# Kernel optimization log

Measured on AMD Instinct MI355X. Metric: run time of the kernel, lower is better.

## Reference

```python
import jax, jax.numpy as jnp
import numpy as np

KH = KW = 3
STRIDE = 1
PAD = 1
DIL = 1


def setup_inputs() -> dict:
    key = jax.random.key(0)
    k0, k1, k2, k3 = jax.random.split(key, 4)
    B, C, H, W = 4, 64, 128, 128
    Cout = 64
    K = KH * KW
    x = jax.random.normal(k0, (B, C, H, W), jnp.float32)
    # main deform-conv weight [Cout, C, KH, KW]
    weight = jax.random.normal(k1, (Cout, C, KH, KW), jnp.float32) * (1.0 / np.sqrt(C * K))
    bias = jax.random.normal(k2, (Cout,), jnp.float32) * 0.01
    # offset-generating conv: 2*K output channels (dy,dx per kernel tap), deform_groups=1
    offset_weight = jax.random.normal(k3, (2 * K, C, KH, KW), jnp.float32) * 0.01
    offset_bias = jnp.zeros((2 * K,), jnp.float32)
    return {"x": x, "weight": weight, "bias": bias,
            "offset_weight": offset_weight, "offset_bias": offset_bias}


def _conv(x, w, b):
    out = jax.lax.conv_general_dilated(
        x, w, (STRIDE, STRIDE), [(PAD, PAD), (PAD, PAD)],
        rhs_dilation=(DIL, DIL), dimension_numbers=("NCHW", "OIHW", "NCHW"))
    return out + b[None, :, None, None]


def _deform_conv(x, weight, bias, offset_weight, offset_bias):
    B, C, H, W = x.shape
    K = KH * KW
    # offsets from sibling conv: [B, 2K, Ho, Wo], layout (k, [dy, dx]) interleaved
    offs = _conv(x, offset_weight, offset_bias)
    Ho, Wo = offs.shape[2], offs.shape[3]
    offs = offs.reshape(B, K, 2, Ho, Wo)
    dy, dx = offs[:, :, 0], offs[:, :, 1]          # [B, K, Ho, Wo]

    # base sampling grid: output pixel origin + dilated kernel tap + learned offset
    base_h = (jnp.arange(Ho) * STRIDE - PAD).astype(x.dtype)
    base_w = (jnp.arange(Wo) * STRIDE - PAD).astype(x.dtype)
    ky, kx = jnp.meshgrid(jnp.arange(KH) * DIL, jnp.arange(KW) * DIL, indexing="ij")
    ky = ky.reshape(K).astype(x.dtype)
    kx = kx.reshape(K).astype(x.dtype)
    py = base_h[None, None, :, None] + ky[None, :, None, None] + dy   # [B,K,Ho,Wo]
    px = base_w[None, None, None, :] + kx[None, :, None, None] + dx

    y0 = jnp.floor(py)
    x0 = jnp.floor(px)
    ly = py - y0   # fractional weights
    lx = px - x0
    y0i = y0.astype(jnp.int32)
    x0i = x0.astype(jnp.int32)

    x_flat = x.reshape(B, C, H * W)

    def gather(yi, xi):
        # zero padding outside the image
        valid = (yi >= 0) & (yi < H) & (xi >= 0) & (xi < W)
        yc = jnp.clip(yi, 0, H - 1)
        xc = jnp.clip(xi, 0, W - 1)
        idx = (yc * W + xc).reshape(B, -1)          # [B, K*Ho*Wo]
        g = jax.vmap(lambda f, i: f[:, i])(x_flat, idx)  # [B, C, K*Ho*Wo]
        g = g.reshape(B, C, K, Ho, Wo)
        return g * valid[:, None].astype(x.dtype)

    v00 = gather(y0i,     x0i)
    v01 = gather(y0i,     x0i + 1)
    v10 = gather(y0i + 1, x0i)
    v11 = gather(y0i + 1, x0i + 1)

    wy = ly[:, None]   # [B,1,K,Ho,Wo]
    wx = lx[:, None]
    patches = (v00 * (1 - wy) * (1 - wx) + v01 * (1 - wy) * wx
               + v10 * wy * (1 - wx) + v11 * wy * wx)   # [B,C,K,Ho,Wo]

    Cout = weight.shape[0]
    out = jnp.einsum("bckhw,ock->bohw", patches, weight.reshape(Cout, C, K))
    return out + bias[None, :, None, None]


def reference(x, weight, bias, offset_weight, offset_bias):
    return _deform_conv(x, weight, bias, offset_weight, offset_bias)
```

## Files before the change

### kernel.cpp

```cpp
#include <hip/hip_runtime.h>

#define B_   4
#define C_   64
#define H_   128
#define W_   128
#define OC_  64
#define K_   9
#define OCH_ 18
#define CK_  576

#define S_    104
#define WCOLS 768
#define XSW   72
#define XSH2  5
#define XSC2  (XSH2*XSW)
#define CHF   (8*XSC2)
#define XSC1  (3*XSW)
#define XSB1  1728
#define XSTOT (2*CHF)
#define NS2   720
#define NS1   432

#define WPAD_HALFS  (OC_*WCOLS)
#define W0PAD_HALFS (32*WCOLS)
#define ZPAGE_BYTE  (2*WPAD_HALFS + 2*W0PAD_HALFS)

using half8v  = __attribute__((ext_vector_type(8))) _Float16;
using half2v  = __attribute__((ext_vector_type(2))) _Float16;
using float4v = __attribute__((ext_vector_type(4))) float;

#define GLDS16(SRC, DST)                                              \
    __builtin_amdgcn_global_load_lds(                                 \
        (__attribute__((address_space(1))) void*)(SRC),               \
        (__attribute__((address_space(3))) void*)(DST), 16, 0, 0)

__global__ void k0_prep(const float* __restrict__ w, const float* __restrict__ ow,
                        _Float16* __restrict__ wpad, _Float16* __restrict__ w0pad,
                        float* __restrict__ zp) {
    if (blockIdx.x == 0 && threadIdx.x < 64) zp[threadIdx.x] = 0.f;
    int i = blockIdx.x * 256 + threadIdx.x;
    if (i < OC_ * WCOLS) {
        int oc = i / WCOLS, col = i - oc * WCOLS;
        int cc = col / 96, r = col - cc * 96;
        int kk = r >> 3, cl = r & 7;
        float v = 0.f;
        if (kk < 9) v = w[oc * CK_ + (cc * 8 + cl) * 9 + kk];
        wpad[i] = (_Float16)v;
    } else {
        int j = i - OC_ * WCOLS;
        if (j < 32 * WCOLS) {
            int rr = j / WCOLS, col = j - rr * WCOLS;
            int cc = col / 96, r = col - cc * 96;
            int kk = r >> 3, cl = r & 7;
            float v = 0.f;
            if (rr < OCH_ && kk < 9) v = ow[rr * CK_ + (cc * 8 + cl) * 9 + kk];
            w0pad[j] = (_Float16)v;
        }
    }
}

__global__ __launch_bounds__(256, 3) void k_fused(
    const float* __restrict__ x, const _Float16* __restrict__ wpad,
    const _Float16* __restrict__ w0pad, const float* __restrict__ bias,
    const float* __restrict__ ob, const float* __restrict__ zp,
    float* __restrict__ out)
{
    __shared__ __align__(16) float    xs[XSTOT];
    __shared__ __align__(16) _Float16 Pl[64 * S_];
    __shared__ float offs_lds[OCH_ * 64];

    const int g   = blockIdx.x;
    const int xcd = g & 7;
    const int n   = g >> 3;
    const int hb  = n & 1;
    const int hol = (n >> 1) & 15;
    const int b   = n >> 5;
    const int ho  = xcd * 16 + hol;

    const int t = threadIdx.x, lane = t & 63, w = t >> 6;
    const int lr = lane & 15, q = lane >> 4;
    const int lpix = w * 16 + lr;
    const int po   = hb * 64 + lpix;
    const int start = hb * 64 - 4;
    const float* xb = x + ((long)b << 20);

    for (int i = t; i < 64 * 12; i += 256) {
        int row = i / 12, j = i - row * 12;
        *(unsigned*)&Pl[row * S_ + 72 + 2 * j] = 0u;
    }

    int g1o[2]; bool g1k[2], g1v[2];
#pragma unroll
    for (int s = 0; s < 2; s++) {
        int idx = t + 256 * s;
        g1v[s] = idx < NS1;
        int ii = g1v[s] ? idx : 0;
        int c  = ii / 54, rj = ii - c * 54;
        int r3 = rj / 18, jc = rj - r3 * 18;
        int gy = ho - 1 + r3, gx = start + 4 * jc;
        g1k[s] = ((unsigned)gy < (unsigned)H_) && (gx >= 0) && (gx + 3 < W_);
        g1o[s] = (c << 14) + (gy << 7) + gx;
    }
    int g2o[3]; bool g2k[3], g2v[3];
#pragma unroll
    for (int s = 0; s < 3; s++) {
        int idx = t + 256 * s;
        g2v[s] = idx < NS2;
        int ii = g2v[s] ? idx : 0;
        int c  = ii / 90, rj = ii - c * 90;
        int r  = rj / 18, jc = rj - r * 18;
        int gy = ho - 2 + r, gx = start + 4 * jc;
        g2k[s] = ((unsigned)gy < (unsigned)H_) && (gx >= 0) && (gx + 3 < W_);
        g2o[s] = (c << 14) + (gy << 7) + gx;
    }

#pragma unroll
    for (int s = 0; s < 2; s++) if (g1v[s])
        GLDS16(g1k[s] ? (xb + g1o[s]) : zp, xs + 4 * (t + 256 * s));

    float4v oa0 = {0.f,0.f,0.f,0.f}, oa1 = {0.f,0.f,0.f,0.f};

    for (int cc = 0; cc < 8; cc++) {
        __syncthreads();
        if (cc < 7) {
            float* dst = xs + ((cc + 1) & 1) * XSB1;
            const float* srcb = xb + ((long)(cc + 1) << 17);
#pragma unroll
            for (int s = 0; s < 2; s++) if (g1v[s])
                GLDS16(g1k[s] ? (srcb + g1o[s]) : zp, dst + 4 * (t + 256 * s));
        }
        {
            const float* b0 = xs + (cc & 1) * XSB1 + (2 * q) * XSC1;
            const float* b1 = b0 + XSC1;
#pragma unroll
            for (int ky = 0; ky < 3; ky++) {
#pragma unroll
                for (int kx = 0; kx < 3; kx++) {
                    float u0 = b0[ky * XSW + lpix + 3 + kx];
                    float u1 = b1[ky * XSW + lpix + 3 + kx];
                    half2v hv = {(_Float16)u0, (_Float16)u1};
                    *(half2v*)&Pl[lpix * S_ + (ky * 3 + kx) * 8 + 2 * q] = hv;
                }
            }
        }
        __syncthreads();
#pragma unroll
        for (int ks = 0; ks < 3; ks++) {
            half8v a0 = *(const half8v*)&w0pad[lr * WCOLS + cc * 96 + ks * 32 + q * 8];
            half8v a1 = *(const half8v*)&w0pad[(16 + lr) * WCOLS + cc * 96 + ks * 32 + q * 8];
            half8v bv = *(const half8v*)&Pl[lpix * S_ + ks * 32 + q * 8];
            oa0 = __builtin_amdgcn_mfma_f32_16x16x32_f16(a0, bv, oa0, 0, 0, 0);
            oa1 = __builtin_amdgcn_mfma_f32_16x16x32_f16(a1, bv, oa1, 0, 0, 0);
        }
    }

#pragma unroll
    for (int r = 0; r < 4; r++) {
        int ch = q * 4 + r;
        offs_lds[ch * 64 + lpix] = oa0[r] + ob[ch];
    }
#pragma unroll
    for (int r = 0; r < 4; r++) {
        int ch = 16 + q * 4 + r;
        if (ch < OCH_) offs_lds[ch * 64 + lpix] = oa1[r] + ob[ch];
    }
    __syncthreads();

#pragma unroll
    for (int s = 0; s < 3; s++) if (g2v[s])
        GLDS16(g2k[s] ? (xb + g2o[s]) : zp, xs + 4 * (t + 256 * s));

    unsigned moff[9];
    float mw0[9], mw1[9], mw2[9], mw3[9];
    unsigned okm = 0;
#pragma unroll
    for (int kk = 0; kk < 9; kk++) {
        int ky = kk / 3, kx = kk - 3 * ky;
        float dy = offs_lds[(2 * kk) * 64 + lpix];
        float dx = offs_lds[(2 * kk + 1) * 64 + lpix];
        float py = (float)(ho - 1 + ky) + dy;
        float px = (float)(po - 1 + kx) + dx;
        float fy = floorf(py), fx = floorf(px);
        float ly = py - fy, lx = px - fx;
        int y0 = (int)fy, x0 = (int)fx;
        int y1 = y0 + 1, x1 = x0 + 1;
        float vy0 = ((unsigned)y0 < (unsigned)H_) ? 1.f : 0.f;
        float vy1 = ((unsigned)y1 < (unsigned)H_) ? 1.f : 0.f;
        float vx0 = ((unsigned)x0 < (unsigned)W_) ? 1.f : 0.f;
        float vx1 = ((unsigned)x1 < (unsigned)W_) ? 1.f : 0.f;
        float w00 = (1.f - ly) * (1.f - lx) * vy0 * vx0;
        float w01 = (1.f - ly) * lx * vy0 * vx1;
        float w10 = ly * (1.f - lx) * vy1 * vx0;
        float w11 = ly * lx * vy1 * vx1;
        int cy0 = min(max(y0, 0), H_ - 1);
        int cy1 = min(max(y1, 0), H_ - 1);
        int xl  = min(max(x0, 0), W_ - 2);
        bool noswap = (x0 == xl);
        mw0[kk] = noswap ? w00 : w01;
        mw1[kk] = noswap ? w01 : w00;
        mw2[kk] = noswap ? w10 : w11;
        mw3[kk] = noswap ? w11 : w10;
        int sy0 = cy0 - (ho - 2);
        int sy1 = cy1 - (ho - 2);
        int sx  = xl - start;
        bool ok = ((unsigned)sy0 < (unsigned)XSH2) && ((unsigned)sy1 < (unsigned)XSH2)
               && ((unsigned)sx < (unsigned)(XSW - 1));
        okm |= (ok ? 1u : 0u) << kk;
        int syc0 = min(max(sy0, 0), XSH2 - 1);
        int syc1 = min(max(sy1, 0), XSH2 - 1);
        int sxc  = min(max(sx, 0), XSW - 2);
        moff[kk] = (unsigned)(syc0 * XSW + sxc) | ((unsigned)(syc1 * XSW + sxc) << 16);
    }
    __syncthreads();

    float4v a00 = {0.f,0.f,0.f,0.f}, a01 = {0.f,0.f,0.f,0.f};
    float4v a10 = {0.f,0.f,0.f,0.f}, a11 = {0.f,0.f,0.f,0.f};
    const int wm = w & 1, wn = w >> 1;

    for (int cc = 0; cc < 8; cc++) {
        if (cc < 7) {
            float* dst = xs + ((cc + 1) & 1) * CHF;
            const float* srcb = xb + ((long)(cc + 1) << 17);
#pragma unroll
            for (int s = 0; s < 3; s++) if (g2v[s])
                GLDS16(g2k[s] ? (srcb + g2o[s]) : zp, dst + 4 * (t + 256 * s));
        }
        {
            const float* x0p = xs + (cc & 1) * CHF + (2 * q) * XSC2;
            const float* x1p = x0p + XSC2;
            const float* xc0 = xb + ((long)(cc * 8 + 2 * q) << 14);
            const float* xc1 = xc0 + (1 << 14);
#pragma unroll
            for (int kk = 0; kk < 9; kk++) {
                int A  = (int)(moff[kk] & 0xFFFFu);
                int Bo = (int)(moff[kk] >> 16);
                float p0 = x0p[A] * mw0[kk] + x0p[A + 1] * mw1[kk]
                         + x0p[Bo] * mw2[kk] + x0p[Bo + 1] * mw3[kk];
                float p1 = x1p[A] * mw0[kk] + x1p[A + 1] * mw1[kk]
                         + x1p[Bo] * mw2[kk] + x1p[Bo + 1] * mw3[kk];
                if (__builtin_expect(!((okm >> kk) & 1u), 0)) {
                    int ky = kk / 3, kx = kk - 3 * ky;
                    float dy = offs_lds[(2 * kk) * 64 + lpix];
                    float dx = offs_lds[(2 * kk + 1) * 64 + lpix];
                    float py = (float)(ho - 1 + ky) + dy;
                    float px = (float)(po - 1 + kx) + dx;
                    int y0 = (int)floorf(py), xq0 = (int)floorf(px);
                    int cy0 = min(max(y0, 0), H_ - 1);
                    int cy1 = min(max(y0 + 1, 0), H_ - 1);
                    int xl  = min(max(xq0, 0), W_ - 2);
                    int ga = (cy0 << 7) + xl, gb = (cy1 << 7) + xl;
                    p0 = xc0[ga] * mw0[kk] + xc0[ga + 1] * mw1[kk]
                       + xc0[gb] * mw2[kk] + xc0[gb + 1] * mw3[kk];
                    p1 = xc1[ga] * mw0[kk] + xc1[ga + 1] * mw1[kk]
                       + xc1[gb] * mw2[kk] + xc1[gb + 1] * mw3[kk];
                }
                half2v hv = {(_Float16)p0, (_Float16)p1};
                *(half2v*)&Pl[lpix * S_ + kk * 8 + 2 * q] = hv;
            }
        }
        __syncthreads();
#pragma unroll
        for (int ks = 0; ks < 3; ks++) {
            half8v A0 = *(const half8v*)&wpad[(wm * 32 + lr) * WCOLS + cc * 96 + ks * 32 + q * 8];
            half8v A1 = *(const half8v*)&wpad[(wm * 32 + 16 + lr) * WCOLS + cc * 96 + ks * 32 + q * 8];
            half8v B0 = *(const half8v*)&Pl[(wn * 32 + lr) * S_ + ks * 32 + q * 8];
            half8v B1 = *(const half8v*)&Pl[(wn * 32 + 16 + lr) * S_ + ks * 32 + q * 8];
            a00 = __builtin_amdgcn_mfma_f32_16x16x32_f16(A0, B0, a00, 0, 0, 0);
            a01 = __builtin_amdgcn_mfma_f32_16x16x32_f16(A0, B1, a01, 0, 0, 0);
            a10 = __builtin_amdgcn_mfma_f32_16x16x32_f16(A1, B0, a10, 0, 0, 0);
            a11 = __builtin_amdgcn_mfma_f32_16x16x32_f16(A1, B1, a11, 0, 0, 0);
        }
        if (cc < 7) __syncthreads();
    }

    const int pixc = hb * 64 + wn * 32 + lr;
#pragma unroll
    for (int r = 0; r < 4; r++) {
        int oc0 = wm * 32 + q * 4 + r;
        int oc1 = oc0 + 16;
        float* o0 = out + (((long)(b * OC_ + oc0)) << 14) + (ho << 7);
        float* o1 = out + (((long)(b * OC_ + oc1)) << 14) + (ho << 7);
        o0[pixc]      = a00[r] + bias[oc0];
        o0[pixc + 16] = a01[r] + bias[oc0];
        o1[pixc]      = a10[r] + bias[oc1];
        o1[pixc + 16] = a11[r] + bias[oc1];
    }
}

extern "C" void kernel_launch(void* const* d_in, const int* in_sizes, int n_in,
                              void* d_out, int out_size, void* d_ws, size_t ws_size,
                              hipStream_t stream) {
    const float* x  = (const float*)d_in[0];
    const float* wt = (const float*)d_in[1];
    const float* bi = (const float*)d_in[2];
    const float* ow = (const float*)d_in[3];
    const float* ob = (const float*)d_in[4];
    float* out = (float*)d_out;

    _Float16* wpad  = (_Float16*)d_ws;
    _Float16* w0pad = wpad + WPAD_HALFS;
    float*    zp    = (float*)((char*)d_ws + ZPAGE_BYTE);

    k0_prep<<<(OC_ * WCOLS + 32 * WCOLS + 255) / 256, 256, 0, stream>>>(wt, ow, wpad, w0pad, zp);
    k_fused<<<B_ * H_ * 2, 256, 0, stream>>>(x, wpad, w0pad, bi, ob, zp, out);
}
```

Before: 156.1 us.

## Pre-pack input into fp16 channel-pair layout and widen sampling window

Adds a prep kernel that converts x into fp16 values interleaved by channel pair, so the fused kernel stages half the bytes into LDS and copies packed pairs straight into the patch buffer without per-element conversion. The halved LDS footprint is spent on a taller sampling window (7 rows instead of 5), which should send fewer deformed samples down the slow global-memory fallback path. The extra prep pass reads all of x and writes an fp16 copy each call. Bilinear sampling now reads fp16-rounded inputs, though the fallback path still reads fp32.

```diff
diff --git a/kernel.cpp b/kernel.cpp
--- a/kernel.cpp
+++ b/kernel.cpp
@@ -12,18 +12,19 @@
 #define S_    104
 #define WCOLS 768
 #define XSW   72
-#define XSH2  5
-#define XSC2  (XSH2*XSW)
-#define CHF   (8*XSC2)
-#define XSC1  (3*XSW)
-#define XSB1  1728
-#define XSTOT (2*CHF)
-#define NS2   720
-#define NS1   432
+#define XSH   7
+#define PWIN2 (XSH*XSW)
+#define PWIN1 (3*XSW)
+#define CH2   (4*PWIN2)
+#define CH1   (4*PWIN1)
+#define XSTOT (2*CH2)
+#define NS1   216
+#define NS2   504
 
 #define WPAD_HALFS  (OC_*WCOLS)
 #define W0PAD_HALFS (32*WCOLS)
 #define ZPAGE_BYTE  (2*WPAD_HALFS + 2*W0PAD_HALFS)
+#define XH_BYTE     (ZPAGE_BYTE + 256)
 
 using half8v  = __attribute__((ext_vector_type(8))) _Float16;
 using half2v  = __attribute__((ext_vector_type(2))) _Float16;
@@ -59,13 +60,31 @@
     }
 }
 
+__global__ void k1_prep(const float* __restrict__ x, unsigned* __restrict__ xh) {
+    int i = blockIdx.x * 256 + threadIdx.x;
+    int bp = i >> 12;
+    int j  = (i & 4095) * 4;
+    int b = bp >> 5, p = bp & 31;
+    const float* c0 = x + (((long)(b * 64 + 2 * p)) << 14) + j;
+    const float* c1 = c0 + (1 << 14);
+    float4v v0 = *(const float4v*)c0;
+    float4v v1 = *(const float4v*)c1;
+    half8v hv;
+#pragma unroll
+    for (int k = 0; k < 4; k++) {
+        hv[2 * k]     = (_Float16)v0[k];
+        hv[2 * k + 1] = (_Float16)v1[k];
+    }
+    *(half8v*)(xh + ((long)bp << 14) + j) = hv;
+}
+
 __global__ __launch_bounds__(256, 3) void k_fused(
-    const float* __restrict__ x, const _Float16* __restrict__ wpad,
-    const _Float16* __restrict__ w0pad, const float* __restrict__ bias,
-    const float* __restrict__ ob, const float* __restrict__ zp,
-    float* __restrict__ out)
+    const float* __restrict__ x, const unsigned* __restrict__ xh,
+    const _Float16* __restrict__ wpad, const _Float16* __restrict__ w0pad,
+    const float* __restrict__ bias, const float* __restrict__ ob,
+    const float* __restrict__ zp, float* __restrict__ out)
 {
-    __shared__ __align__(16) float    xs[XSTOT];
+    __shared__ __align__(16) unsigned xs1[XSTOT];
     __shared__ __align__(16) _Float16 Pl[64 * S_];
     __shared__ float offs_lds[OCH_ * 64];
 
@@ -82,64 +101,56 @@
     const int lpix = w * 16 + lr;
     const int po   = hb * 64 + lpix;
     const int start = hb * 64 - 4;
-    const float* xb = x + ((long)b << 20);
+    const float*    xb  = x  + ((long)b << 20);
+    const unsigned* xhb = xh + ((long)b << 19);
+    const unsigned* zpu = (const unsigned*)zp;
 
     for (int i = t; i < 64 * 12; i += 256) {
         int row = i / 12, j = i - row * 12;
         *(unsigned*)&Pl[row * S_ + 72 + 2 * j] = 0u;
     }
 
-    int g1o[2]; bool g1k[2], g1v[2];
-#pragma unroll
-    for (int s = 0; s < 2; s++) {
-        int idx = t + 256 * s;
-        g1v[s] = idx < NS1;
-        int ii = g1v[s] ? idx : 0;
-        int c  = ii / 54, rj = ii - c * 54;
+    int g1o; bool g1k; const bool g1v = t < NS1;
+    {
+        int ii = g1v ? t : 0;
+        int pr = ii / 54, rj = ii - pr * 54;
         int r3 = rj / 18, jc = rj - r3 * 18;
         int gy = ho - 1 + r3, gx = start + 4 * jc;
-        g1k[s] = ((unsigned)gy < (unsigned)H_) && (gx >= 0) && (gx + 3 < W_);
-        g1o[s] = (c << 14) + (gy << 7) + gx;
-    }
-    int g2o[3]; bool g2k[3], g2v[3];
-#pragma unroll
-    for (int s = 0; s < 3; s++) {
+        g1k = ((unsigned)gy < (unsigned)H_) && (gx >= 0) && (gx + 3 < W_);
+        g1o = (pr << 14) + (gy << 7) + gx;
+    }
+    int g2o[2]; bool g2k[2], g2v[2];
+#pragma unroll
+    for (int s = 0; s < 2; s++) {
         int idx = t + 256 * s;
         g2v[s] = idx < NS2;
         int ii = g2v[s] ? idx : 0;
-        int c  = ii / 90, rj = ii - c * 90;
+        int pr = ii / 126, rj = ii - pr * 126;
         int r  = rj / 18, jc = rj - r * 18;
-        int gy = ho - 2 + r, gx = start + 4 * jc;
+        int gy = ho - 3 + r, gx = start + 4 * jc;
         g2k[s] = ((unsigned)gy < (unsigned)H_) && (gx >= 0) && (gx + 3 < W_);
-        g2o[s] = (c << 14) + (gy << 7) + gx;
-    }
-
-#pragma unroll
-    for (int s = 0; s < 2; s++) if (g1v[s])
-        GLDS16(g1k[s] ? (xb + g1o[s]) : zp, xs + 4 * (t + 256 * s));
+        g2o[s] = (pr << 14) + (gy << 7) + gx;
+    }
+
+    if (g1v) GLDS16(g1k ? (xhb + g1o) : zpu, xs1 + 4 * t);
 
     float4v oa0 = {0.f,0.f,0.f,0.f}, oa1 = {0.f,0.f,0.f,0.f};
 
     for (int cc = 0; cc < 8; cc++) {
         __syncthreads();
         if (cc < 7) {
-            float* dst = xs + ((cc + 1) & 1) * XSB1;
-            const float* srcb = xb + ((long)(cc + 1) << 17);
-#pragma unroll
-            for (int s = 0; s < 2; s++) if (g1v[s])
-                GLDS16(g1k[s] ? (srcb + g1o[s]) : zp, dst + 4 * (t + 256 * s));
+            unsigned* dst = xs1 + ((cc + 1) & 1) * CH1;
+            const unsigned* srcb = xhb + ((long)(cc + 1) << 16);
+            if (g1v) GLDS16(g1k ? (srcb + g1o) : zpu, dst + 4 * t);
         }
         {
-            const float* b0 = xs + (cc & 1) * XSB1 + (2 * q) * XSC1;
-            const float* b1 = b0 + XSC1;
+            const unsigned* b0 = xs1 + (cc & 1) * CH1 + q * PWIN1;
 #pragma unroll
             for (int ky = 0; ky < 3; ky++) {
 #pragma unroll
                 for (int kx = 0; kx < 3; kx++) {
-                    float u0 = b0[ky * XSW + lpix + 3 + kx];
-                    float u1 = b1[ky * XSW + lpix + 3 + kx];
-                    half2v hv = {(_Float16)u0, (_Float16)u1};
-                    *(half2v*)&Pl[lpix * S_ + (ky * 3 + kx) * 8 + 2 * q] = hv;
+                    *(unsigned*)&Pl[lpix * S_ + (ky * 3 + kx) * 8 + 2 * q] =
+                        b0[ky * XSW + lpix + 3 + kx];
                 }
             }
         }
@@ -167,8 +178,8 @@
     __syncthreads();
 
 #pragma unroll
-    for (int s = 0; s < 3; s++) if (g2v[s])
-        GLDS16(g2k[s] ? (xb + g2o[s]) : zp, xs + 4 * (t + 256 * s));
+    for (int s = 0; s < 2; s++) if (g2v[s])
+        GLDS16(g2k[s] ? (xhb + g2o[s]) : zpu, xs1 + 4 * (t + 256 * s));
 
     unsigned moff[9];
     float mw0[9], mw1[9], mw2[9], mw3[9];
@@ -200,14 +211,14 @@
         mw1[kk] = noswap ? w01 : w00;
         mw2[kk] = noswap ? w10 : w11;
         mw3[kk] = noswap ? w11 : w10;
-        int sy0 = cy0 - (ho - 2);
-        int sy1 = cy1 - (ho - 2);
+        int sy0 = cy0 - (ho - 3);
+        int sy1 = cy1 - (ho - 3);
         int sx  = xl - start;
-        bool ok = ((unsigned)sy0 < (unsigned)XSH2) && ((unsigned)sy1 < (unsigned)XSH2)
+        bool ok = ((unsigned)sy0 < (unsigned)XSH) && ((unsigned)sy1 < (unsigned)XSH)
                && ((unsigned)sx < (unsigned)(XSW - 1));
         okm |= (ok ? 1u : 0u) << kk;
-        int syc0 = min(max(sy0, 0), XSH2 - 1);
-        int syc1 = min(max(sy1, 0), XSH2 - 1);
+        int syc0 = min(max(sy0, 0), XSH - 1);
+        int syc1 = min(max(sy1, 0), XSH - 1);
         int sxc  = min(max(sx, 0), XSW - 2);
         moff[kk] = (unsigned)(syc0 * XSW + sxc) | ((unsigned)(syc1 * XSW + sxc) << 16);
     }
@@ -219,25 +230,26 @@
 
     for (int cc = 0; cc < 8; cc++) {
         if (cc < 7) {
-            float* dst = xs + ((cc + 1) & 1) * CHF;
-            const float* srcb = xb + ((long)(cc + 1) << 17);
-#pragma unroll
-            for (int s = 0; s < 3; s++) if (g2v[s])
-                GLDS16(g2k[s] ? (srcb + g2o[s]) : zp, dst + 4 * (t + 256 * s));
+            unsigned* dst = xs1 + ((cc + 1) & 1) * CH2;
+            const unsigned* srcb = xhb + ((long)(cc + 1) << 16);
+#pragma unroll
+            for (int s = 0; s < 2; s++) if (g2v[s])
+                GLDS16(g2k[s] ? (srcb + g2o[s]) : zpu, dst + 4 * (t + 256 * s));
         }
         {
-            const float* x0p = xs + (cc & 1) * CHF + (2 * q) * XSC2;
-            const float* x1p = x0p + XSC2;
+            const half2v* bp = (const half2v*)(xs1 + (cc & 1) * CH2) + q * PWIN2;
             const float* xc0 = xb + ((long)(cc * 8 + 2 * q) << 14);
             const float* xc1 = xc0 + (1 << 14);
 #pragma unroll
             for (int kk = 0; kk < 9; kk++) {
                 int A  = (int)(moff[kk] & 0xFFFFu);
                 int Bo = (int)(moff[kk] >> 16);
-                float p0 = x0p[A] * mw0[kk] + x0p[A + 1] * mw1[kk]
-                         + x0p[Bo] * mw2[kk] + x0p[Bo + 1] * mw3[kk];
-                float p1 = x1p[A] * mw0[kk] + x1p[A + 1] * mw1[kk]
-                         + x1p[Bo] * mw2[kk] + x1p[Bo + 1] * mw3[kk];
+                half2v d00 = bp[A],  d01 = bp[A + 1];
+                half2v d10 = bp[Bo], d11 = bp[Bo + 1];
+                float p0 = (float)d00[0] * mw0[kk] + (float)d01[0] * mw1[kk]
+                         + (float)d10[0] * mw2[kk] + (float)d11[0] * mw3[kk];
+                float p1 = (float)d00[1] * mw0[kk] + (float)d01[1] * mw1[kk]
+                         + (float)d10[1] * mw2[kk] + (float)d11[1] * mw3[kk];
                 if (__builtin_expect(!((okm >> kk) & 1u), 0)) {
                     int ky = kk / 3, kx = kk - 3 * ky;
                     float dy = offs_lds[(2 * kk) * 64 + lpix];
@@ -300,7 +312,9 @@
     _Float16* wpad  = (_Float16*)d_ws;
     _Float16* w0pad = wpad + WPAD_HALFS;
     float*    zp    = (float*)((char*)d_ws + ZPAGE_BYTE);
+    unsigned* xh    = (unsigned*)((char*)d_ws + XH_BYTE);
 
     k0_prep<<<(OC_ * WCOLS + 32 * WCOLS + 255) / 256, 256, 0, stream>>>(wt, ow, wpad, w0pad, zp);
-    k_fused<<<B_ * H_ * 2, 256, 0, stream>>>(x, wpad, w0pad, bi, ob, zp, out);
+    k1_prep<<<2048, 256, 0, stream>>>(x, xh);
+    k_fused<<<B_ * H_ * 2, 256, 0, stream>>>(x, xh, wpad, w0pad, bi, ob, zp, out);
 }
```

New measurement: 159.3 us. 2.1% more time.
